# Kernel tuning notes

Hardware: AMD Instinct MI355X
Metric: run time of the kernel (lower is better)

The kernel has to match this reference:

```python
import jax, jax.numpy as jnp
import numpy as np

B, L, D = 4, 1536, 768
H, DQK, DV = 8, 64, 96
NPF = 96  # num_pos_feats = (DV // (2*3)) * (2*3)


def pos_feats_exponential(positions, feature_size, seq_length, min_half_life=3.0):
    # positions: (P, 1); returns (P, feature_size)
    max_range = jnp.log(seq_length) / jnp.log(2.0)
    half_life = jnp.power(2.0, jnp.linspace(min_half_life, max_range, feature_size))
    return jnp.exp(-jnp.log(2.0) / half_life * jnp.abs(positions))


def pos_feats_central_mask(positions, feature_size):
    center_widths = jnp.power(2.0, jnp.arange(1, feature_size + 1, dtype=jnp.float32)) - 1.0
    return (center_widths > jnp.abs(positions)).astype(jnp.float32)


def pos_feats_gamma(positions, feature_size, seq_length):
    stddev = seq_length / (2.0 * feature_size)
    start_mean = seq_length / feature_size
    mean = jnp.linspace(start_mean, seq_length, feature_size)
    concentration = (mean / stddev) ** 2
    rate = mean / (stddev ** 2)
    x = jnp.abs(positions)
    log_unnorm = jax.scipy.special.xlogy(concentration - 1.0, x) - rate * x
    log_norm = jax.scipy.special.gammaln(concentration) - concentration * jnp.log(rate)
    probs = jnp.exp(log_unnorm - log_norm) + 1e-8
    return probs / jnp.max(probs, axis=0, keepdims=True)


def pos_feats_all(positions, feature_size, seq_length, symmetric=False):
    # 3 feature functions; if asymmetric, each is doubled by a signed copy
    num_basis = feature_size // 6
    emb = jnp.concatenate([
        pos_feats_exponential(positions, num_basis, seq_length),
        pos_feats_central_mask(positions, num_basis),
        pos_feats_gamma(positions, num_basis, seq_length),
    ], axis=-1)
    if not symmetric:
        emb = jnp.concatenate([emb, jnp.sign(positions) * emb], axis=-1)
    return emb  # (P, feature_size)


def relative_shift(x):
    # x: (b, h, t1, 2*t1 - 1) -> (b, h, t1, t1), Transformer-XL shift trick
    b, h, t1, t2 = x.shape
    x = jnp.concatenate([jnp.zeros_like(x[..., :1]), x], axis=-1)  # pad -> width t2+1 == 2*t1
    x = x.reshape(b, h, t2 + 1, t1)[:, :, 1:, :]
    x = x.reshape(b, h, t1, t2)
    return x[..., : (t2 + 2) // 2]


def setup_inputs() -> dict:
    key = jax.random.key(0)
    ks = jax.random.split(key, 9)

    def vs(k, shape):  # VarianceScaling(scale=2.0), fan_in on leading dim for 2D
        fan_in = shape[0] if len(shape) == 2 else shape[-1]
        return jax.random.normal(k, shape, jnp.float32) * np.float32(np.sqrt(2.0 / fan_in))

    return {
        "x": jax.random.normal(ks[0], (B, L, D), jnp.float32),
        "Q_w": vs(ks[1], (D, H * DQK)),
        "K_w": vs(ks[2], (D, H * DQK)),
        "V_w": vs(ks[3], (D, H * DV)),
        "out_w": vs(ks[4], (D, H * DV)),
        "out_b": jnp.zeros((H * DV,), jnp.float32),
        "rel_K_w": vs(ks[5], (NPF, H * DQK)),
        "r_w_bias": vs(ks[6], (1, H, 1, DQK)),
        "r_r_bias": vs(ks[7], (1, H, 1, DQK)),
    }


def reference(x, Q_w, K_w, V_w, out_w, out_b, rel_K_w, r_w_bias, r_r_bias):
    b, l, d = x.shape
    h = r_w_bias.shape[1]
    dqk = Q_w.shape[1] // h

    def heads(w, inp):
        out = inp @ w  # (b, t, h*dh)
        return out.reshape(inp.shape[0], inp.shape[1], h, -1).transpose(0, 2, 1, 3)

    Q = heads(Q_w, x) * (dqk ** -0.5)  # scaling=True
    K = heads(K_w, x)
    V = heads(V_w, x)

    positions = jnp.arange(1 - l, l, dtype=jnp.float32)[:, None]       # (2l-1, 1)
    pe = pos_feats_all(positions, rel_K_w.shape[0], float(l))           # (2l-1, npf)
    r_K = (pe @ rel_K_w).reshape(2 * l - 1, h, dqk).transpose(1, 0, 2)  # (h, 2l-1, dqk)

    content = jnp.einsum('bhid,bhjd->bhij', Q + r_w_bias, K)            # (b, h, l, l)
    rel = jnp.einsum('bhid,hjd->bhij', Q + r_r_bias, r_K)               # (b, h, l, 2l-1)
    logits = content + relative_shift(rel)

    w = jax.nn.softmax(logits, axis=-1)
    attn = jnp.einsum('bhij,bhjd->bhid', w, V)                          # (b, h, l, dv)
    out = attn.transpose(0, 2, 1, 3).reshape(b, l, -1) @ out_w + out_b
    return out
```

## Files before the change

kernel.cpp:

```cpp
#include <hip/hip_runtime.h>


typedef unsigned short u16;
typedef unsigned int   u32;

typedef __bf16 bf16x8_t __attribute__((ext_vector_type(8)));
typedef unsigned short u16x8_t __attribute__((ext_vector_type(8)));
typedef float f32x4_t __attribute__((ext_vector_type(4)));

union Frag { u16x8_t u; bf16x8_t b; };

__device__ __forceinline__ float bf2f(u16 v){
  union { u32 i; float f; } c; c.i = ((u32)v) << 16; return c.f;
}
__device__ __forceinline__ u16 f2bf(float f){
  union { float f; u32 i; } c; c.f = f;
  u32 r = c.i + 0x7FFFu + ((c.i >> 16) & 1u);
  return (u16)(r >> 16);
}

#define GLB __attribute__((address_space(1)))
#define LDSAS __attribute__((address_space(3)))
__device__ __forceinline__ void async16(const void* g, void* l){
  __builtin_amdgcn_global_load_lds((const GLB u32*)g, (LDSAS u32*)l, 16, 0, 0);
}

#define LQ   1536
#define NPOS 3071
#define NPOSP 3072

__global__ void cvt_x(const float* __restrict__ x, u16* __restrict__ xb)
{
  int gid = blockIdx.x * 256 + threadIdx.x;
  float4 v = ((const float4*)x)[gid];
  xb[4*gid+0] = f2bf(v.x); xb[4*gid+1] = f2bf(v.y);
  xb[4*gid+2] = f2bf(v.z); xb[4*gid+3] = f2bf(v.w);
}

__global__ __launch_bounds__(256) void transpose_w(
    const float* __restrict__ Qw_, const float* __restrict__ Kw_,
    const float* __restrict__ Vw_, const float* __restrict__ Ow_,
    u16* __restrict__ WtQKV, u16* __restrict__ WtOut)
{
  __shared__ u16 tile[64][65];
  int bx = blockIdx.x;
  const float* src; int stride, cl0, c0, k0; u16* dst;
  if (bx < 336) {
    int ct = bx % 28, kt = bx / 28;
    c0 = ct*64; k0 = kt*64;
    if (c0 < 512)       { src = Qw_; stride = 512; cl0 = c0; }
    else if (c0 < 1024) { src = Kw_; stride = 512; cl0 = c0 - 512; }
    else                { src = Vw_; stride = 768; cl0 = c0 - 1024; }
    dst = WtQKV;
  } else {
    int b2 = bx - 336; int ct = b2 % 12, kt = b2 / 12;
    c0 = ct*64; k0 = kt*64; src = Ow_; stride = 768; cl0 = c0; dst = WtOut;
  }
  int t = threadIdx.x;
  #pragma unroll
  for (int e = 0; e < 16; ++e) {
    int idx = e*256 + t; int row = idx >> 6, col = idx & 63;
    tile[row][col] = f2bf(src[(size_t)(k0 + row)*stride + cl0 + col]);
  }
  __syncthreads();
  #pragma unroll
  for (int e = 0; e < 16; ++e) {
    int idx = e*256 + t; int orow = idx >> 6, ocol = idx & 63;
    dst[(size_t)(c0 + orow)*768 + k0 + ocol] = tile[ocol][orow];
  }
}

__global__ void gamma_max_k(float* __restrict__ gmax)
{
  int f = blockIdx.x;
  float fi   = (float)(f + 1);
  float conc = 4.0f * fi * fi;
  float rate = fi / 24.0f;
  float c1   = conc - 1.0f;
  float lognorm = lgammaf(conc) - conc * logf(rate);
  float mx = 0.0f;
  for (int x = threadIdx.x; x < 1536; x += 256) {
    float xf = (float)x;
    float lu = (x == 0) ? -INFINITY : (c1 * logf(xf) - rate * xf);
    float p  = expf(lu - lognorm) + 1e-8f;
    mx = fmaxf(mx, p);
  }
  for (int d = 1; d < 64; d <<= 1) mx = fmaxf(mx, __shfl_xor(mx, d, 64));
  __shared__ float red[4];
  if ((threadIdx.x & 63) == 0) red[threadIdx.x >> 6] = mx;
  __syncthreads();
  if (threadIdx.x == 0)
    gmax[f] = fmaxf(fmaxf(red[0], red[1]), fmaxf(red[2], red[3]));
}

__global__ void rk_k(const float* __restrict__ gmax,
                     const float* __restrict__ relKw, u16* __restrict__ rK)
{
  int k = blockIdx.x;
  int t = threadIdx.x;
  if (k == NPOS) {
    for (int c = t; c < 512; c += 256)
      rK[(((size_t)(c >> 6))*NPOSP + NPOS)*64 + (c & 63)] = 0;
    return;
  }
  __shared__ float feats[96];
  float pos = (float)(k - (LQ - 1));
  float x   = fabsf(pos);
  float sgn = (float)((pos > 0.0f) - (pos < 0.0f));
  if (t < 96) {
    int tb = (t < 48) ? t : t - 48;
    float val;
    if (tb < 16) {
      float max_range = log2f((float)LQ);
      float hl = exp2f(3.0f + (float)tb * (max_range - 3.0f) / 15.0f);
      val = expf(-0.69314718056f / hl * x);
    } else if (tb < 32) {
      int i = tb - 16;
      float width = (float)(1u << (i + 1)) - 1.0f;
      val = (width > x) ? 1.0f : 0.0f;
    } else {
      int i = tb - 32;
      float fi   = (float)(i + 1);
      float conc = 4.0f * fi * fi;
      float rate = fi / 24.0f;
      float lognorm = lgammaf(conc) - conc * logf(rate);
      float lu = (x == 0.0f) ? -INFINITY : ((conc - 1.0f) * logf(x) - rate * x);
      float p  = expf(lu - lognorm) + 1e-8f;
      val = p / gmax[i];
    }
    feats[t] = (t < 48) ? val : sgn * val;
  }
  __syncthreads();
  for (int c = t; c < 512; c += 256) {
    float acc = 0.0f;
    #pragma unroll 8
    for (int f = 0; f < 96; ++f) acc += feats[f] * relKw[(size_t)f*512 + c];
    rK[(((size_t)(c >> 6))*NPOSP + k)*64 + (c & 63)] = f2bf(acc);
  }
}

__global__ __launch_bounds__(256) void qkv_gemm(
    const u16* __restrict__ xb, const u16* __restrict__ Wt,
    u16* __restrict__ Qb, u16* __restrict__ Kc, u16* __restrict__ Vt)
{
  const int n0 = blockIdx.x * 64;
  const int m0 = blockIdx.y * 64;
  const int tid = threadIdx.x, w = tid >> 6, lane = tid & 63, q = lane >> 4, s = lane & 15;

  __shared__ __align__(16) u16 At[64*64];
  __shared__ __align__(16) u16 Bt[64*64];

  const char* ag = (const char*)(xb + (size_t)m0 * 768);
  const char* bg = (const char*)(Wt + (size_t)n0 * 768);

  const f32x4_t fz = {0.f, 0.f, 0.f, 0.f};
  f32x4_t acc[4] = {fz, fz, fz, fz};

  for (int kk = 0; kk < 768; kk += 64) {
    #pragma unroll
    for (int c = 0; c < 2; ++c) {
      int ck = w*128 + c*64 + lane;
      int grow = ck >> 3, gcol = (ck & 7) ^ (grow & 7);
      async16(ag + (size_t)grow*1536 + (size_t)(kk + gcol*8)*2, &At[(size_t)(w*128 + c*64)*8]);
      async16(bg + (size_t)grow*1536 + (size_t)(kk + gcol*8)*2, &Bt[(size_t)(w*128 + c*64)*8]);
    }
    __syncthreads();
    #pragma unroll
    for (int kf = 0; kf < 2; ++kf) {
      int sw = (kf*4 + q) ^ (s & 7);
      Frag af; af.u = *(const u16x8_t*)&At[(size_t)((16*w + s)*8 + sw)*8];
      #pragma unroll
      for (int ns = 0; ns < 4; ++ns) {
        Frag bf; bf.u = *(const u16x8_t*)&Bt[(size_t)((ns*16 + s)*8 + sw)*8];
        acc[ns] = __builtin_amdgcn_mfma_f32_16x16x32_bf16(af.b, bf.b, acc[ns], 0, 0, 0);
      }
    }
    __syncthreads();
  }

  #pragma unroll
  for (int ns = 0; ns < 4; ++ns) {
    int c = n0 + ns*16 + s;
    #pragma unroll
    for (int r = 0; r < 4; ++r) {
      int row = m0 + 16*w + q*4 + r;
      int b = row / LQ, i = row - b*LQ;
      float v = acc[ns][r];
      if (c < 512) {
        int h = c >> 6, d = c & 63;
        Qb[(((size_t)(b*8 + h))*LQ + i)*64 + d] = f2bf(v * 0.125f);
      } else if (c < 1024) {
        int cc = c - 512, h = cc >> 6, d = cc & 63;
        Kc[(((size_t)(b*8 + h))*LQ + i)*64 + d] = f2bf(v);
      } else {
        int cc = c - 1024, h = cc / 96, vv = cc - h*96;
        Vt[(((size_t)(b*8 + h))*96 + vv)*LQ + i] = f2bf(v);
      }
    }
  }
}

__global__ __launch_bounds__(512, 4) void attn_k(
    const u16* __restrict__ Qb, const u16* __restrict__ Kc,
    const u16* __restrict__ Vt, const u16* __restrict__ rK,
    const float* __restrict__ rwb, const float* __restrict__ rrb,
    u16* __restrict__ attnO, u16* __restrict__ Opart, float* __restrict__ ml,
    int nz)
{
  const int n = blockIdx.x;
  const int bpb = 12 * nz;
  const int slot = n >> 3;
  const int bh = (n & 7) * 4 + slot / bpb;
  const int rm = slot % bpb;
  const int it = rm % 12, z = rm / 12;
  const int i0 = it * 128;
  const int b = bh >> 3, h = bh & 7;
  const int tid = threadIdx.x;
  const int w = tid >> 6, lane = tid & 63, q = lane >> 4, s = lane & 15;

  __shared__ __align__(16) u16 Kt[64*64];
  __shared__ __align__(16) u16 Rt[192*64];
  __shared__ __align__(16) u16 Vs[96*64];
  __shared__ __align__(16) u16 Ps[8][16][72];

  Frag qwf[2], qrf[2];
  {
    const u16* qb = Qb + (((size_t)bh)*LQ + i0 + 16*w + s)*64;
    #pragma unroll
    for (int kf = 0; kf < 2; ++kf) {
      u16x8_t qraw = *(const u16x8_t*)(qb + kf*32 + q*8);
      #pragma unroll
      for (int j = 0; j < 8; ++j) {
        int d = kf*32 + q*8 + j;
        float qv = bf2f(qraw[j]);
        qwf[kf].u[j] = f2bf(qv + rwb[h*64 + d]);
        qrf[kf].u[j] = f2bf(qv + rrb[h*64 + d]);
      }
    }
  }

  const f32x4_t fz = {0.f, 0.f, 0.f, 0.f};
  float mrun[4], lrun[4];
  f32x4_t acco[6];
  #pragma unroll
  for (int r = 0; r < 4; ++r) { mrun[r] = -1e30f; lrun[r] = 0.f; }
  #pragma unroll
  for (int vs = 0; vs < 6; ++vs) acco[vs] = fz;

  const char* kcb = (const char*)(Kc + ((size_t)bh)*LQ*64);
  const char* vtb = (const char*)(Vt + ((size_t)bh)*96*LQ);
  const char* rkb = (const char*)(rK + ((size_t)h)*NPOSP*64);

  const int swz0 = (0*4 + q) ^ (s & 7);
  const int swz1 = (1*4 + q) ^ (s & 7);

  const int njt = 24 / nz;
  const int jt0 = z * njt;

  for (int jt = jt0; jt < jt0 + njt; ++jt) {
    const int j0 = jt * 64;
    const int k0 = j0 - i0 + (LQ - 128);

    {
      const char* kg = kcb + (size_t)j0 * 128;
      {
        int ck = tid;
        int grow = ck >> 3, gcol = (ck & 7) ^ (grow & 7);
        async16(kg + (size_t)grow*128 + gcol*16, &Kt[(size_t)(w*64)*8]);
      }
      const char* rg = rkb + (size_t)k0 * 128;
      #pragma unroll
      for (int c = 0; c < 3; ++c) {
        int ck = c*512 + tid;
        int grow = ck >> 3, gcol = (ck & 7) ^ (grow & 7);
        async16(rg + (size_t)grow*128 + gcol*16, &Rt[(size_t)(c*512 + w*64)*8]);
      }
      const char* vg = vtb + (size_t)j0 * 2;
      {
        int ck = tid;
        int grow = ck >> 3, gcol = (ck & 7) ^ (grow & 7);
        async16(vg + (size_t)grow*(LQ*2) + gcol*16, &Vs[(size_t)(w*64)*8]);
      }
      if (tid < 256) {
        int ck = 512 + tid;
        int grow = ck >> 3, gcol = (ck & 7) ^ (grow & 7);
        async16(vg + (size_t)grow*(LQ*2) + gcol*16, &Vs[(size_t)(512 + w*64)*8]);
      }
    }
    __syncthreads();

    f32x4_t accc[4] = {fz, fz, fz, fz};
    #pragma unroll
    for (int ns = 0; ns < 4; ++ns) {
      int row = ns*16 + s;
      Frag b0; b0.u = *(const u16x8_t*)&Kt[(size_t)(row*8 + swz0)*8];
      Frag b1; b1.u = *(const u16x8_t*)&Kt[(size_t)(row*8 + swz1)*8];
      accc[ns] = __builtin_amdgcn_mfma_f32_16x16x32_bf16(qwf[0].b, b0.b, accc[ns], 0, 0, 0);
      accc[ns] = __builtin_amdgcn_mfma_f32_16x16x32_bf16(qwf[1].b, b1.b, accc[ns], 0, 0, 0);
    }

    f32x4_t accr[5] = {fz, fz, fz, fz, fz};
    #pragma unroll
    for (int nn = 0; nn < 5; ++nn) {
      int row = (7 - w + nn)*16 + s;
      Frag b0; b0.u = *(const u16x8_t*)&Rt[(size_t)(row*8 + swz0)*8];
      Frag b1; b1.u = *(const u16x8_t*)&Rt[(size_t)(row*8 + swz1)*8];
      accr[nn] = __builtin_amdgcn_mfma_f32_16x16x32_bf16(qrf[0].b, b0.b, accr[nn], 0, 0, 0);
      accr[nn] = __builtin_amdgcn_mfma_f32_16x16x32_bf16(qrf[1].b, b1.b, accr[nn], 0, 0, 0);
    }

    #pragma unroll
    for (int r = 0; r < 4; ++r) {
      int tt = s + 15 - 4*q - r;
      int srcl = (lane & 48) | (tt & 15);
      bool hi = tt >= 16;
      float v[5];
      #pragma unroll
      for (int nn = 0; nn < 5; ++nn) v[nn] = __shfl(accr[nn][r], srcl, 64);
      #pragma unroll
      for (int ns = 0; ns < 4; ++ns)
        accc[ns][r] += hi ? v[ns + 1] : v[ns];
    }

    #pragma unroll
    for (int r = 0; r < 4; ++r) {
      float mx = fmaxf(fmaxf(accc[0][r], accc[1][r]), fmaxf(accc[2][r], accc[3][r]));
      for (int d = 1; d < 16; d <<= 1) mx = fmaxf(mx, __shfl_xor(mx, d, 64));
      float mnew  = fmaxf(mrun[r], mx);
      float alpha = __expf(mrun[r] - mnew);
      float sum = 0.f;
      #pragma unroll
      for (int ns = 0; ns < 4; ++ns) {
        float p = __expf(accc[ns][r] - mnew);
        accc[ns][r] = p; sum += p;
      }
      for (int d = 1; d < 16; d <<= 1) sum += __shfl_xor(sum, d, 64);
      mrun[r] = mnew;
      lrun[r] = lrun[r]*alpha + sum;
      #pragma unroll
      for (int vs = 0; vs < 6; ++vs) acco[vs][r] *= alpha;
    }

    #pragma unroll
    for (int ns = 0; ns < 4; ++ns)
      #pragma unroll
      for (int r = 0; r < 4; ++r)
        Ps[w][q*4 + r][ns*16 + s] = f2bf(accc[ns][r]);

    #pragma unroll
    for (int kf = 0; kf < 2; ++kf) {
      Frag pf; pf.u = *(const u16x8_t*)(&Ps[w][s][kf*32 + q*8]);
      int sw = kf ? swz1 : swz0;
      #pragma unroll
      for (int vs = 0; vs < 6; ++vs) {
        int row = vs*16 + s;
        Frag vf; vf.u = *(const u16x8_t*)&Vs[(size_t)(row*8 + sw)*8];
        acco[vs] = __builtin_amdgcn_mfma_f32_16x16x32_bf16(pf.b, vf.b, acco[vs], 0, 0, 0);
      }
    }
    __syncthreads();
  }

  if (nz == 1) {
    #pragma unroll
    for (int vs = 0; vs < 6; ++vs) {
      int v = vs*16 + s;
      #pragma unroll
      for (int r = 0; r < 4; ++r) {
        int i = i0 + 16*w + q*4 + r;
        attnO[((size_t)b*LQ + i)*768 + h*96 + v] = f2bf(acco[vs][r] / lrun[r]);
      }
    }
  } else {
    #pragma unroll
    for (int vs = 0; vs < 6; ++vs) {
      int v = vs*16 + s;
      #pragma unroll
      for (int r = 0; r < 4; ++r) {
        int i = i0 + 16*w + q*4 + r;
        size_t rg = (size_t)(z*32 + bh)*LQ + i;
        Opart[rg*96 + v] = f2bf(acco[vs][r]);
      }
    }
    if (s == 0) {
      #pragma unroll
      for (int r = 0; r < 4; ++r) {
        int i = i0 + 16*w + q*4 + r;
        size_t rg = (size_t)(z*32 + bh)*LQ + i;
        ml[rg*2 + 0] = mrun[r];
        ml[rg*2 + 1] = lrun[r];
      }
    }
  }
}

__global__ void combine_k(const u16* __restrict__ Opart, const float* __restrict__ ml,
                          u16* __restrict__ attnO, int nz)
{
  int g = blockIdx.x * 256 + threadIdx.x;
  if (g >= 32*LQ*96) return;
  int v = g % 96, row = g / 96;
  int bh = row / LQ, i = row - bh*LQ;
  int b = bh >> 3, h = bh & 7;
  float M = -1e30f;
  for (int z = 0; z < nz; ++z)
    M = fmaxf(M, ml[((size_t)(z*32 + bh)*LQ + i)*2]);
  float L = 0.f, num = 0.f;
  for (int z = 0; z < nz; ++z) {
    size_t rg = (size_t)(z*32 + bh)*LQ + i;
    float e = __expf(ml[rg*2] - M);
    L   += ml[rg*2 + 1] * e;
    num += bf2f(Opart[rg*96 + v]) * e;
  }
  attnO[((size_t)b*LQ + i)*768 + h*96 + v] = f2bf(num / L);
}

__global__ __launch_bounds__(256) void out_gemm(
    const u16* __restrict__ A, const u16* __restrict__ Wt,
    const float* __restrict__ bias, float* __restrict__ out)
{
  const int n0 = blockIdx.x * 64;
  const int m0 = blockIdx.y * 64;
  const int tid = threadIdx.x, w = tid >> 6, lane = tid & 63, q = lane >> 4, s = lane & 15;

  __shared__ __align__(16) u16 At[64*64];
  __shared__ __align__(16) u16 Bt[64*64];

  const char* ag = (const char*)(A  + (size_t)m0 * 768);
  const char* bg = (const char*)(Wt + (size_t)n0 * 768);

  const f32x4_t fz = {0.f, 0.f, 0.f, 0.f};
  f32x4_t acc[4] = {fz, fz, fz, fz};

  for (int kk = 0; kk < 768; kk += 64) {
    #pragma unroll
    for (int c = 0; c < 2; ++c) {
      int ck = w*128 + c*64 + lane;
      int grow = ck >> 3, gcol = (ck & 7) ^ (grow & 7);
      async16(ag + (size_t)grow*1536 + (size_t)(kk + gcol*8)*2, &At[(size_t)(w*128 + c*64)*8]);
      async16(bg + (size_t)grow*1536 + (size_t)(kk + gcol*8)*2, &Bt[(size_t)(w*128 + c*64)*8]);
    }
    __syncthreads();
    #pragma unroll
    for (int kf = 0; kf < 2; ++kf) {
      int sw = (kf*4 + q) ^ (s & 7);
      Frag af; af.u = *(const u16x8_t*)&At[(size_t)((16*w + s)*8 + sw)*8];
      #pragma unroll
      for (int ns = 0; ns < 4; ++ns) {
        Frag bf; bf.u = *(const u16x8_t*)&Bt[(size_t)((ns*16 + s)*8 + sw)*8];
        acc[ns] = __builtin_amdgcn_mfma_f32_16x16x32_bf16(af.b, bf.b, acc[ns], 0, 0, 0);
      }
    }
    __syncthreads();
  }

  #pragma unroll
  for (int ns = 0; ns < 4; ++ns) {
    int c = n0 + ns*16 + s;
    float bv = bias[c];
    #pragma unroll
    for (int r = 0; r < 4; ++r) {
      int row = m0 + 16*w + q*4 + r;
      out[(size_t)row*768 + c] = acc[ns][r] + bv;
    }
  }
}

extern "C" void kernel_launch(void* const* d_in, const int* in_sizes, int n_in,
                              void* d_out, int out_size, void* d_ws, size_t ws_size,
                              hipStream_t stream)
{
  (void)out_size;

  static const int dict_sig[9] = {4718592,393216,393216,589824,589824,768,49152,512,512};
  bool is_dict = (n_in == 9);
  for (int i = 0; i < 9 && i < n_in; ++i)
    if (in_sizes[i] != dict_sig[i]) is_dict = false;

  const float *x, *Qw_w, *Kw_w, *Vw_w, *Ow_w, *out_b, *relKw, *rwb, *rrb;
  if (is_dict) {
    x     = (const float*)d_in[0];  Qw_w  = (const float*)d_in[1];
    Kw_w  = (const float*)d_in[2];  Vw_w  = (const float*)d_in[3];
    Ow_w  = (const float*)d_in[4];  out_b = (const float*)d_in[5];
    relKw = (const float*)d_in[6];  rwb   = (const float*)d_in[7];
    rrb   = (const float*)d_in[8];
  } else {
    const float* p393[2] = {nullptr,nullptr}; int n393 = 0;
    const float* p589[2] = {nullptr,nullptr}; int n589 = 0;
    const float* p512[2] = {nullptr,nullptr}; int n512 = 0;
    const float *px = nullptr, *prel = nullptr, *pb = nullptr;
    for (int i = 0; i < n_in; ++i) {
      const float* p = (const float*)d_in[i];
      switch (in_sizes[i]) {
        case 4718592: px = p; break;
        case 49152:   prel = p; break;
        case 768:     pb = p; break;
        case 393216:  if (n393 < 2) p393[n393++] = p; break;
        case 589824:  if (n589 < 2) p589[n589++] = p; break;
        case 512:     if (n512 < 2) p512[n512++] = p; break;
        default: break;
      }
    }
    x = px; relKw = prel; out_b = pb;
    Qw_w = p393[0]; Kw_w = p393[1];
    Vw_w = p589[0]; Ow_w = p589[1];
    rwb  = p512[0]; rrb  = p512[1];
  }

  float* out = (float*)d_out;

  char* ws = (char*)d_ws;
  size_t off = 0;
  auto alloc = [&](size_t bytes) -> void* {
    void* p = ws + off;
    off += (bytes + 255) & ~(size_t)255;
    return p;
  };

  float* gmax  = (float*)alloc(256);
  u16*   WtQKV = (u16*)  alloc((size_t)1792*768*2);
  u16*   WtOut = (u16*)  alloc((size_t)768*768*2);
  u16*   rK    = (u16*)  alloc((size_t)8*NPOSP*64*2);
  u16*   Qb    = (u16*)  alloc((size_t)32*LQ*64*2);
  u16*   Kc    = (u16*)  alloc((size_t)32*LQ*64*2);
  u16*   Vt    = (u16*)  alloc((size_t)32*96*LQ*2);
  u16*   xb    = (u16*)  alloc((size_t)6144*768*2);
  u16*   attnO = xb;

  size_t base_off = off;
  auto need = [&](int nzv) -> size_t {
    size_t o = base_off;
    o += (((size_t)nzv*32*LQ*96*2) + 255) & ~(size_t)255;
    o += (((size_t)nzv*32*LQ*2*4) + 255) & ~(size_t)255;
    return o;
  };
  int nz = 1;
  if (ws_size >= need(4)) nz = 4;
  else if (ws_size >= need(2)) nz = 2;
  u16*   Opart = nullptr; float* ml = nullptr;
  if (nz > 1) {
    Opart = (u16*)  alloc((size_t)nz*32*LQ*96*2);
    ml    = (float*)alloc((size_t)nz*32*LQ*2*4);
  }

  cvt_x      <<<dim3(4608), dim3(256), 0, stream>>>(x, xb);
  transpose_w<<<dim3(480),  dim3(256), 0, stream>>>(Qw_w, Kw_w, Vw_w, Ow_w, WtQKV, WtOut);
  gamma_max_k<<<dim3(16),   dim3(256), 0, stream>>>(gmax);
  rk_k       <<<dim3(NPOSP),dim3(256), 0, stream>>>(gmax, relKw, rK);
  qkv_gemm   <<<dim3(28,96),dim3(256), 0, stream>>>(xb, WtQKV, Qb, Kc, Vt);
  attn_k     <<<dim3(384*nz),dim3(512), 0, stream>>>(Qb, Kc, Vt, rK, rwb, rrb,
                                                     attnO, Opart, ml, nz);
  if (nz > 1)
    combine_k<<<dim3(18432), dim3(256), 0, stream>>>(Opart, ml, attnO, nz);
  out_gemm   <<<dim3(12,96),dim3(256), 0, stream>>>(attnO, WtOut, out_b, out);
}
```

Baseline: 341.9 us.

## Double-buffer K, relative-K and V tiles in attention kernel LDS

Splits the LDS tiles for K, rel-K and V into two buffers and issues the async global-to-LDS loads for the next key tile before computing on the current one, so memory latency overlaps the MFMA work. Launch bounds drop from 4 to 2 blocks per CU because LDS use roughly doubles, which lowers occupancy. The single __syncthreads at the end of each iteration now has to cover both the prefetch completion and buffer reuse; correctness depends on the async loads being waited on by that barrier.

New measurement: 371.1 us. +8.5%, slower.

```diff
diff --git a/kernel.cpp b/kernel.cpp
--- a/kernel.cpp
+++ b/kernel.cpp
@@ -200,7 +200,7 @@
   }
 }
 
-__global__ __launch_bounds__(512, 4) void attn_k(
+__global__ __launch_bounds__(512, 2) void attn_k(
     const u16* __restrict__ Qb, const u16* __restrict__ Kc,
     const u16* __restrict__ Vt, const u16* __restrict__ rK,
     const float* __restrict__ rwb, const float* __restrict__ rrb,
@@ -218,9 +218,9 @@
   const int tid = threadIdx.x;
   const int w = tid >> 6, lane = tid & 63, q = lane >> 4, s = lane & 15;
 
-  __shared__ __align__(16) u16 Kt[64*64];
-  __shared__ __align__(16) u16 Rt[192*64];
-  __shared__ __align__(16) u16 Vs[96*64];
+  __shared__ __align__(16) u16 Kt[2][64*64];
+  __shared__ __align__(16) u16 Rt[2][192*64];
+  __shared__ __align__(16) u16 Vs[2][96*64];
   __shared__ __align__(16) u16 Ps[8][16][72];
 
   Frag qwf[2], qrf[2];
@@ -257,44 +257,55 @@
   const int njt = 24 / nz;
   const int jt0 = z * njt;
 
+  auto stage = [&](int bi, int jtS) {
+    const int j0S = jtS * 64;
+    const int k0S = j0S - i0 + (LQ - 128);
+    u16* KtB = &Kt[bi][0];
+    u16* RtB = &Rt[bi][0];
+    u16* VsB = &Vs[bi][0];
+    const char* kg = kcb + (size_t)j0S * 128;
+    {
+      int ck = tid;
+      int grow = ck >> 3, gcol = (ck & 7) ^ (grow & 7);
+      async16(kg + (size_t)grow*128 + gcol*16, &KtB[(size_t)(w*64)*8]);
+    }
+    const char* rg = rkb + (size_t)k0S * 128;
+    #pragma unroll
+    for (int c = 0; c < 3; ++c) {
+      int ck = c*512 + tid;
+      int grow = ck >> 3, gcol = (ck & 7) ^ (grow & 7);
+      async16(rg + (size_t)grow*128 + gcol*16, &RtB[(size_t)(c*512 + w*64)*8]);
+    }
+    const char* vg = vtb + (size_t)j0S * 2;
+    {
+      int ck = tid;
+      int grow = ck >> 3, gcol = (ck & 7) ^ (grow & 7);
+      async16(vg + (size_t)grow*(LQ*2) + gcol*16, &VsB[(size_t)(w*64)*8]);
+    }
+    if (tid < 256) {
+      int ck = 512 + tid;
+      int grow = ck >> 3, gcol = (ck & 7) ^ (grow & 7);
+      async16(vg + (size_t)grow*(LQ*2) + gcol*16, &VsB[(size_t)(512 + w*64)*8]);
+    }
+  };
+
+  stage(0, jt0);
+  __syncthreads();
+
+  int cur = 0;
   for (int jt = jt0; jt < jt0 + njt; ++jt) {
-    const int j0 = jt * 64;
-    const int k0 = j0 - i0 + (LQ - 128);
-
-    {
-      const char* kg = kcb + (size_t)j0 * 128;
-      {
-        int ck = tid;
-        int grow = ck >> 3, gcol = (ck & 7) ^ (grow & 7);
-        async16(kg + (size_t)grow*128 + gcol*16, &Kt[(size_t)(w*64)*8]);
-      }
-      const char* rg = rkb + (size_t)k0 * 128;
-      #pragma unroll
-      for (int c = 0; c < 3; ++c) {
-        int ck = c*512 + tid;
-        int grow = ck >> 3, gcol = (ck & 7) ^ (grow & 7);
-        async16(rg + (size_t)grow*128 + gcol*16, &Rt[(size_t)(c*512 + w*64)*8]);
-      }
-      const char* vg = vtb + (size_t)j0 * 2;
-      {
-        int ck = tid;
-        int grow = ck >> 3, gcol = (ck & 7) ^ (grow & 7);
-        async16(vg + (size_t)grow*(LQ*2) + gcol*16, &Vs[(size_t)(w*64)*8]);
-      }
-      if (tid < 256) {
-        int ck = 512 + tid;
-        int grow = ck >> 3, gcol = (ck & 7) ^ (grow & 7);
-        async16(vg + (size_t)grow*(LQ*2) + gcol*16, &Vs[(size_t)(512 + w*64)*8]);
-      }
-    }
-    __syncthreads();
+    if (jt + 1 < jt0 + njt) stage(cur ^ 1, jt + 1);
+
+    const u16* KtC = &Kt[cur][0];
+    const u16* RtC = &Rt[cur][0];
+    const u16* VsC = &Vs[cur][0];
 
     f32x4_t accc[4] = {fz, fz, fz, fz};
     #pragma unroll
     for (int ns = 0; ns < 4; ++ns) {
       int row = ns*16 + s;
-      Frag b0; b0.u = *(const u16x8_t*)&Kt[(size_t)(row*8 + swz0)*8];
-      Frag b1; b1.u = *(const u16x8_t*)&Kt[(size_t)(row*8 + swz1)*8];
+      Frag b0; b0.u = *(const u16x8_t*)&KtC[(size_t)(row*8 + swz0)*8];
+      Frag b1; b1.u = *(const u16x8_t*)&KtC[(size_t)(row*8 + swz1)*8];
       accc[ns] = __builtin_amdgcn_mfma_f32_16x16x32_bf16(qwf[0].b, b0.b, accc[ns], 0, 0, 0);
       accc[ns] = __builtin_amdgcn_mfma_f32_16x16x32_bf16(qwf[1].b, b1.b, accc[ns], 0, 0, 0);
     }
@@ -303,8 +314,8 @@
     #pragma unroll
     for (int nn = 0; nn < 5; ++nn) {
       int row = (7 - w + nn)*16 + s;
-      Frag b0; b0.u = *(const u16x8_t*)&Rt[(size_t)(row*8 + swz0)*8];
-      Frag b1; b1.u = *(const u16x8_t*)&Rt[(size_t)(row*8 + swz1)*8];
+      Frag b0; b0.u = *(const u16x8_t*)&RtC[(size_t)(row*8 + swz0)*8];
+      Frag b1; b1.u = *(const u16x8_t*)&RtC[(size_t)(row*8 + swz1)*8];
       accr[nn] = __builtin_amdgcn_mfma_f32_16x16x32_bf16(qrf[0].b, b0.b, accr[nn], 0, 0, 0);
       accr[nn] = __builtin_amdgcn_mfma_f32_16x16x32_bf16(qrf[1].b, b1.b, accr[nn], 0, 0, 0);
     }
@@ -354,11 +365,13 @@
       #pragma unroll
       for (int vs = 0; vs < 6; ++vs) {
         int row = vs*16 + s;
-        Frag vf; vf.u = *(const u16x8_t*)&Vs[(size_t)(row*8 + sw)*8];
+        Frag vf; vf.u = *(const u16x8_t*)&VsC[(size_t)(row*8 + sw)*8];
         acco[vs] = __builtin_amdgcn_mfma_f32_16x16x32_bf16(pf.b, vf.b, acco[vs], 0, 0, 0);
       }
     }
+
     __syncthreads();
+    cur ^= 1;
   }
 
   if (nz == 1) {
```

## Ring-buffer relative-key tiles, prefetch next K/R/V tiles, sum probabilities via MFMA

Applied to the files above, without the earlier changes.

The relative-position key buffer becomes a 256-row circular buffer. Each iteration now loads only the 64 new rows instead of re-staging 192. The next iteration's K and R tiles are issued right after the score MFMAs, and the next V tile right after the PV MFMAs, so global-to-LDS copies overlap compute instead of sitting at the top of the loop. The softmax row-sum shuffle reduction is replaced by an extra MFMA of the bf16 probabilities against a ones vector. This makes the normaliser come from bf16-rounded P, which is consistent with the numerator but slightly changes rounding.

New measurement: 328.4 us. 1.04x faster.

```diff
diff --git a/kernel.cpp b/kernel.cpp
--- a/kernel.cpp
+++ b/kernel.cpp
@@ -219,7 +219,7 @@
   const int w = tid >> 6, lane = tid & 63, q = lane >> 4, s = lane & 15;
 
   __shared__ __align__(16) u16 Kt[64*64];
-  __shared__ __align__(16) u16 Rt[192*64];
+  __shared__ __align__(16) u16 Rt[256*64];
   __shared__ __align__(16) u16 Vs[96*64];
   __shared__ __align__(16) u16 Ps[8][16][72];
 
@@ -239,13 +239,18 @@
     }
   }
 
+  Frag ones;
+  #pragma unroll
+  for (int j = 0; j < 8; ++j) ones.u[j] = 0x3F80;
+
   const f32x4_t fz = {0.f, 0.f, 0.f, 0.f};
-  float mrun[4], lrun[4];
-  f32x4_t acco[6];
-  #pragma unroll
-  for (int r = 0; r < 4; ++r) { mrun[r] = -1e30f; lrun[r] = 0.f; }
+  float mrun[4];
+  f32x4_t acco[6], accl;
+  #pragma unroll
+  for (int r = 0; r < 4; ++r) mrun[r] = -1e30f;
   #pragma unroll
   for (int vs = 0; vs < 6; ++vs) acco[vs] = fz;
+  accl = fz;
 
   const char* kcb = (const char*)(Kc + ((size_t)bh)*LQ*64);
   const char* vtb = (const char*)(Vt + ((size_t)bh)*96*LQ);
@@ -256,38 +261,45 @@
 
   const int njt = 24 / nz;
   const int jt0 = z * njt;
-
-  for (int jt = jt0; jt < jt0 + njt; ++jt) {
-    const int j0 = jt * 64;
-    const int k0 = j0 - i0 + (LQ - 128);
-
+  const int jtend = jt0 + njt;
+
+  auto stageK = [&](int jtS) {
+    const char* kg = kcb + (size_t)(jtS*64) * 128;
+    int ck = tid;
+    int grow = ck >> 3, gcol = (ck & 7) ^ (grow & 7);
+    async16(kg + (size_t)grow*128 + gcol*16, &Kt[(size_t)(w*64)*8]);
+  };
+  auto stageV = [&](int jtS) {
+    const char* vg = vtb + (size_t)(jtS*64) * 2;
     {
-      const char* kg = kcb + (size_t)j0 * 128;
-      {
-        int ck = tid;
-        int grow = ck >> 3, gcol = (ck & 7) ^ (grow & 7);
-        async16(kg + (size_t)grow*128 + gcol*16, &Kt[(size_t)(w*64)*8]);
-      }
-      const char* rg = rkb + (size_t)k0 * 128;
-      #pragma unroll
-      for (int c = 0; c < 3; ++c) {
-        int ck = c*512 + tid;
-        int grow = ck >> 3, gcol = (ck & 7) ^ (grow & 7);
-        async16(rg + (size_t)grow*128 + gcol*16, &Rt[(size_t)(c*512 + w*64)*8]);
-      }
-      const char* vg = vtb + (size_t)j0 * 2;
-      {
-        int ck = tid;
-        int grow = ck >> 3, gcol = (ck & 7) ^ (grow & 7);
-        async16(vg + (size_t)grow*(LQ*2) + gcol*16, &Vs[(size_t)(w*64)*8]);
-      }
-      if (tid < 256) {
-        int ck = 512 + tid;
-        int grow = ck >> 3, gcol = (ck & 7) ^ (grow & 7);
-        async16(vg + (size_t)grow*(LQ*2) + gcol*16, &Vs[(size_t)(512 + w*64)*8]);
-      }
-    }
-    __syncthreads();
+      int ck = tid;
+      int grow = ck >> 3, gcol = (ck & 7) ^ (grow & 7);
+      async16(vg + (size_t)grow*(LQ*2) + gcol*16, &Vs[(size_t)(w*64)*8]);
+    }
+    if (tid < 256) {
+      int ck = 512 + tid;
+      int grow = ck >> 3, gcol = (ck & 7) ^ (grow & 7);
+      async16(vg + (size_t)grow*(LQ*2) + gcol*16, &Vs[(size_t)(512 + w*64)*8]);
+    }
+  };
+  auto stageR64 = [&](int ar0) {
+    const char* rg = rkb + (size_t)ar0 * 128;
+    int ck = tid;
+    int grow = ck >> 3, gcol = (ck & 7) ^ (grow & 7);
+    async16(rg + (size_t)grow*128 + gcol*16, &Rt[(size_t)((ar0 & 255) + w*8)*64]);
+  };
+
+  {
+    const int k00 = jt0*64 - i0 + (LQ - 128);
+    stageK(jt0);
+    stageR64(k00); stageR64(k00 + 64); stageR64(k00 + 128);
+    stageV(jt0);
+  }
+  __syncthreads();
+
+  for (int jt = jt0; jt < jtend; ++jt) {
+    const int k0 = jt*64 - i0 + (LQ - 128);
+    const int kb = k0 & 255;
 
     f32x4_t accc[4] = {fz, fz, fz, fz};
     #pragma unroll
@@ -302,11 +314,18 @@
     f32x4_t accr[5] = {fz, fz, fz, fz, fz};
     #pragma unroll
     for (int nn = 0; nn < 5; ++nn) {
-      int row = (7 - w + nn)*16 + s;
+      int row = (kb + (7 - w + nn)*16 + s) & 255;
       Frag b0; b0.u = *(const u16x8_t*)&Rt[(size_t)(row*8 + swz0)*8];
       Frag b1; b1.u = *(const u16x8_t*)&Rt[(size_t)(row*8 + swz1)*8];
       accr[nn] = __builtin_amdgcn_mfma_f32_16x16x32_bf16(qrf[0].b, b0.b, accr[nn], 0, 0, 0);
       accr[nn] = __builtin_amdgcn_mfma_f32_16x16x32_bf16(qrf[1].b, b1.b, accr[nn], 0, 0, 0);
+    }
+
+    __syncthreads();
+
+    if (jt + 1 < jtend) {
+      stageK(jt + 1);
+      stageR64(k0 + 192);
     }
 
     #pragma unroll
@@ -328,15 +347,11 @@
       for (int d = 1; d < 16; d <<= 1) mx = fmaxf(mx, __shfl_xor(mx, d, 64));
       float mnew  = fmaxf(mrun[r], mx);
       float alpha = __expf(mrun[r] - mnew);
-      float sum = 0.f;
-      #pragma unroll
-      for (int ns = 0; ns < 4; ++ns) {
-        float p = __expf(accc[ns][r] - mnew);
-        accc[ns][r] = p; sum += p;
-      }
-      for (int d = 1; d < 16; d <<= 1) sum += __shfl_xor(sum, d, 64);
+      #pragma unroll
+      for (int ns = 0; ns < 4; ++ns)
+        accc[ns][r] = __expf(accc[ns][r] - mnew);
       mrun[r] = mnew;
-      lrun[r] = lrun[r]*alpha + sum;
+      accl[r] *= alpha;
       #pragma unroll
       for (int vs = 0; vs < 6; ++vs) acco[vs][r] *= alpha;
     }
@@ -357,8 +372,12 @@
         Frag vf; vf.u = *(const u16x8_t*)&Vs[(size_t)(row*8 + sw)*8];
         acco[vs] = __builtin_amdgcn_mfma_f32_16x16x32_bf16(pf.b, vf.b, acco[vs], 0, 0, 0);
       }
-    }
+      accl = __builtin_amdgcn_mfma_f32_16x16x32_bf16(pf.b, ones.b, accl, 0, 0, 0);
+    }
+
     __syncthreads();
+
+    if (jt + 1 < jtend) stageV(jt + 1);
   }
 
   if (nz == 1) {
@@ -368,7 +387,7 @@
       #pragma unroll
       for (int r = 0; r < 4; ++r) {
         int i = i0 + 16*w + q*4 + r;
-        attnO[((size_t)b*LQ + i)*768 + h*96 + v] = f2bf(acco[vs][r] / lrun[r]);
+        attnO[((size_t)b*LQ + i)*768 + h*96 + v] = f2bf(acco[vs][r] / accl[r]);
       }
     }
   } else {
@@ -388,7 +407,7 @@
         int i = i0 + 16*w + q*4 + r;
         size_t rg = (size_t)(z*32 + bh)*LQ + i;
         ml[rg*2 + 0] = mrun[r];
-        ml[rg*2 + 1] = lrun[r];
+        ml[rg*2 + 1] = accl[r];
       }
     }
   }
```
